# Kernel tuning notes

Hardware: AMD Instinct MI355X
Metric: run time of the kernel (lower is better)

Reference implementation:

```python
import jax, jax.numpy as jnp
import numpy as np

VOCAB, D, B, S, L, K = 50000, 256, 128, 64, 32, 32
EPS = 1e-12  # tf.nn.l2_normalize epsilon


def setup_inputs() -> dict:
    key = jax.random.key(0)
    ks = jax.random.split(key, 7)
    prgrph = jax.random.randint(ks[0], (B, S, L), 0, VOCAB, dtype=jnp.int32)
    prgrph_mask = jax.random.randint(ks[1], (B, S, L), 0, 2, dtype=jnp.int32).astype(bool)
    keys = jax.random.normal(ks[2], (B, K, D), dtype=jnp.float32)
    embedding_matrix = jax.random.normal(ks[3], (VOCAB, D), dtype=jnp.float32) * 0.05
    U = jax.random.normal(ks[4], (D, D), dtype=jnp.float32) * 0.05
    V = jax.random.normal(ks[5], (D, D), dtype=jnp.float32) * 0.05
    W = jax.random.normal(ks[6], (D, D), dtype=jnp.float32) * 0.05
    return {"prgrph": prgrph, "prgrph_mask": prgrph_mask, "keys": keys,
            "embedding_matrix": embedding_matrix, "U": U, "V": V, "W": W}


def reference(prgrph, prgrph_mask, keys, embedding_matrix, U, V, W):
    # bag-of-words sentence encoding: [B, S, L, D] -> sum over words -> [B, S, D]
    enc_sents = embedding_matrix[prgrph].sum(axis=2)
    sent_mask = prgrph_mask[:, :, 0]  # [B, S] sentence availability

    h0 = jnp.zeros_like(keys)  # initial entity hidden state [B, K, D]

    def step(h, inp):
        e, m = inp  # e: [B, D], m: [B] bool
        # gate_i = sigmoid(sum_d e * (h_i + k_i))  -> [B, K]
        gate = jax.nn.sigmoid(jnp.einsum('bd,bkd->bk', e, h + keys))
        # h_tilda = relu(h U + k V + e W)  -> [B, K, D]
        h_tilda = jax.nn.relu(
            jnp.einsum('bkd,de->bke', h, U)
            + jnp.einsum('bkd,de->bke', keys, V)
            + (e @ W)[:, None, :]
        )
        upd = h + gate[..., None] * h_tilda
        upd = upd * jax.lax.rsqrt(jnp.maximum((upd * upd).sum(-1, keepdims=True), EPS))
        h_new = jnp.where(m[:, None, None], upd, h)  # masked rows keep prev state
        return h_new, None

    h_final, _ = jax.lax.scan(step, h0, (enc_sents.transpose(1, 0, 2), sent_mask.T))
    return h_final  # [B, K, D]
```

## Files before the change

### kernel.cpp

```cpp
#include <hip/hip_runtime.h>

#define D 256
#define B 128
#define S 64
#define L 32
#define K 32
#define KH 16
#define NW 8
#define NSUB 2
#define HSTR 260

typedef _Float16 f16x8 __attribute__((ext_vector_type(8)));
typedef float f32x4 __attribute__((ext_vector_type(4)));
typedef unsigned short u16;

__device__ __forceinline__ u16 h_bits(_Float16 h) {
    union { _Float16 h; u16 u; } x; x.h = h; return x.u;
}

__global__ __launch_bounds__(256) void mask_kernel(const void* mraw, int* mask_out) {
    __shared__ int flag;
    const int tid = threadIdx.x;
    if (tid == 0) flag = 0;
    __syncthreads();
    const unsigned int* w32 = (const unsigned int*)mraw;
    int loc = 0;
    #pragma unroll
    for (int j = 0; j < 4; ++j)
        if (w32[tid * 4 + j] > 1u) loc = 1;
    if (loc) flag = 1;
    __syncthreads();
    const bool is_bytes = (flag != 0);
    const unsigned char* b8 = (const unsigned char*)mraw;
    const int* i32 = (const int*)mraw;
    const int i = blockIdx.x * 256 + tid;
    mask_out[i] = is_bytes ? (int)b8[(size_t)i * L] : i32[(size_t)i * L];
}

__global__ __launch_bounds__(256) void pre_kernel(
    const int* __restrict__ prgrph, const float* __restrict__ E,
    const float* __restrict__ Wm, const float* __restrict__ Vm,
    const float* __restrict__ keys, const int* __restrict__ mask,
    float* __restrict__ enc, float* __restrict__ eW,
    float* __restrict__ keysV, float* __restrict__ ek) {
    const int t = threadIdx.x, wave = t >> 6, lane = t & 63;
    __shared__ int   sidx[32][L];
    __shared__ float a_s[32][264];
    __shared__ float ks[32][260];

    const float* Bm;
    float* O;

    if (blockIdx.x < (B * S) / 32) {
        const int bid = blockIdx.x;
        const int b = bid >> 1;

        #pragma unroll
        for (int j = 0; j < 4; ++j) {
            const int idx = t * 4 + j;
            sidx[idx >> 5][idx & 31] = prgrph[(size_t)bid * 1024 + idx];
        }
        __syncthreads();

        const float4* E4 = (const float4*)E;
        for (int sl = wave * 8; sl < wave * 8 + 8; ++sl) {
            if (!mask[bid * 32 + sl]) continue;
            float4 a = make_float4(0.f, 0.f, 0.f, 0.f);
            #pragma unroll
            for (int l = 0; l < L; ++l) {
                const float4 v = E4[(size_t)sidx[sl][l] * (D / 4) + lane];
                a.x += v.x; a.y += v.y; a.z += v.z; a.w += v.w;
            }
            *(float4*)&a_s[sl][lane * 4] = a;
            *(float4*)&enc[(size_t)(bid * 32 + sl) * D + lane * 4] = a;
        }
        __syncthreads();
        Bm = Wm;
        O = eW + (size_t)bid * 32 * D;
    } else {
        const int row0 = (blockIdx.x - (B * S) / 32) * 32;
        const float4* Ag = (const float4*)(keys + (size_t)row0 * D);
        for (int i = t; i < 32 * D / 4; i += 256) {
            const float4 v = Ag[i];
            *(float4*)&a_s[i >> 6][(i & 63) * 4] = v;
        }
        __syncthreads();
        Bm = Vm;
        O = keysV + (size_t)row0 * D;
    }

    {
        const int r0 = wave * 8, c0 = lane * 4;
        float4 acc[8];
        #pragma unroll
        for (int i = 0; i < 8; ++i) acc[i] = make_float4(0.f, 0.f, 0.f, 0.f);
        for (int d = 0; d < D; d += 4) {
            float4 av[8];
            #pragma unroll
            for (int i = 0; i < 8; ++i) av[i] = *(const float4*)&a_s[r0 + i][d];
            #pragma unroll
            for (int j = 0; j < 4; ++j) {
                const float4 w = *(const float4*)(Bm + (size_t)(d + j) * D + c0);
                #pragma unroll
                for (int i = 0; i < 8; ++i) {
                    const float a = (j == 0) ? av[i].x : (j == 1) ? av[i].y
                                  : (j == 2) ? av[i].z : av[i].w;
                    acc[i].x += a * w.x; acc[i].y += a * w.y;
                    acc[i].z += a * w.z; acc[i].w += a * w.w;
                }
            }
        }
        #pragma unroll
        for (int i = 0; i < 8; ++i)
            *(float4*)&O[(size_t)(r0 + i) * D + c0] = acc[i];
    }

    if (blockIdx.x >= (B * S) / 32) return;

    {
        const int bid = blockIdx.x;
        const int b = bid >> 1;
        const float4* kg = (const float4*)(keys + (size_t)b * K * D);
        for (int i = t; i < K * D / 4; i += 256) {
            const float4 v = kg[i];
            *(float4*)&ks[i >> 6][(i & 63) * 4] = v;
        }
        __syncthreads();
        const int sl = t >> 3, kq = t & 7;
        if (mask[bid * 32 + sl]) {
            float acc[4];
            #pragma unroll
            for (int j = 0; j < 4; ++j) acc[j] = 0.f;
            for (int d4 = 0; d4 < D / 4; ++d4) {
                const float4 e = *(const float4*)&a_s[sl][d4 * 4];
                #pragma unroll
                for (int j = 0; j < 4; ++j) {
                    const float4 kv = *(const float4*)&ks[kq + 8 * j][d4 * 4];
                    acc[j] += e.x * kv.x + e.y * kv.y + e.z * kv.z + e.w * kv.w;
                }
            }
            #pragma unroll
            for (int j = 0; j < 4; ++j)
                ek[(size_t)(bid * 32 + sl) * K + kq + 8 * j] = acc[j];
        }
    }
}

__global__ __launch_bounds__(512, 2) void recur_kernel(
    const float* __restrict__ enc, const float* __restrict__ eWp,
    const float* __restrict__ keysV, const float* __restrict__ ek,
    const float* __restrict__ U, const int* __restrict__ mask,
    float* __restrict__ out) {
    const int b  = blockIdx.x >> 1;
    const int kh = (blockIdx.x & 1) * KH;
    const int t = threadIdx.x;
    const int wave = t >> 6, lane = t & 63;
    const int n = lane & 15, quad = lane >> 4;

    __shared__ u16 hF[2][KH][HSTR];
    __shared__ float redN[2][KH][NW];
    __shared__ float redG[2][KH][NW];

    f16x8 Uhi[NSUB][8], Ulo[NSUB][8];
    #pragma unroll
    for (int sub = 0; sub < NSUB; ++sub) {
        const int col = wave * 32 + sub * 16 + n;
        #pragma unroll
        for (int kt = 0; kt < 8; ++kt) {
            #pragma unroll
            for (int j = 0; j < 8; ++j) {
                const int k = kt * 32 + quad * 8 + j;
                const float u = U[(size_t)k * D + col];
                const _Float16 uh = (_Float16)u;
                Uhi[sub][kt][j] = uh;
                Ulo[sub][kt][j] = (_Float16)(u - (float)uh);
            }
        }
    }
    #pragma unroll
    for (int sub = 0; sub < NSUB; ++sub)
        #pragma unroll
        for (int kt = 0; kt < 8; ++kt)
            asm volatile("" : "+a"(Uhi[sub][kt]), "+a"(Ulo[sub][kt]));

    float upv[4][NSUB];
    float rn[4];
    float keysVc[4][NSUB];
    #pragma unroll
    for (int reg = 0; reg < 4; ++reg) {
        rn[reg] = 1.f;
        const size_t base = (size_t)(b * K + kh + quad * 4 + reg) * D;
        #pragma unroll
        for (int sub = 0; sub < NSUB; ++sub) {
            upv[reg][sub] = 0.f;
            keysVc[reg][sub] = keysV[base + wave * 32 + sub * 16 + n];
        }
    }

    const int* bm = mask + b * S;
    unsigned long long rem = __ballot(bm[lane & 63] != 0);

    float eWc[NSUB];
    float4 ekv = make_float4(0.f, 0.f, 0.f, 0.f);
    #pragma unroll
    for (int sub = 0; sub < NSUB; ++sub) eWc[sub] = 0.f;
    if (rem) {
        const int s0 = (int)__builtin_ctzll(rem);
        const size_t eo = (size_t)(b * S + s0) * D;
        #pragma unroll
        for (int sub = 0; sub < NSUB; ++sub)
            eWc[sub] = eWp[eo + wave * 32 + sub * 16 + n];
        ekv = *(const float4*)(ek + (size_t)(b * S + s0) * K + kh + quad * 4);
    }

    int p = 0, q = 0;
    bool first = true;
    while (rem) {
        rem &= rem - 1;
        const int sn = rem ? (int)__builtin_ctzll(rem) : -1;

        float e_n[NSUB];
        #pragma unroll
        for (int sub = 0; sub < NSUB; ++sub) e_n[sub] = 0.f;
        if (sn >= 0) {
            const size_t eo = (size_t)(b * S + sn) * D;
            #pragma unroll
            for (int sub = 0; sub < NSUB; ++sub)
                e_n[sub] = enc[eo + wave * 32 + sub * 16 + n];
        }

        f32x4 acc[NSUB][2];
        #pragma unroll
        for (int sub = 0; sub < NSUB; ++sub) {
            acc[sub][0] = (f32x4){0.f, 0.f, 0.f, 0.f};
            acc[sub][1] = (f32x4){0.f, 0.f, 0.f, 0.f};
        }
        if (!first) {
            #pragma unroll
            for (int kt = 0; kt < 8; ++kt) {
                const f16x8 av = *(const f16x8*)&hF[p][n][kt * 32 + quad * 8];
                #pragma unroll
                for (int sub = 0; sub < NSUB; ++sub) {
                    acc[sub][0] = __builtin_amdgcn_mfma_f32_16x16x32_f16(av, Uhi[sub][kt], acc[sub][0], 0, 0, 0);
                    acc[sub][1] = __builtin_amdgcn_mfma_f32_16x16x32_f16(av, Ulo[sub][kt], acc[sub][1], 0, 0, 0);
                }
            }
        }

        float gate[4];
        #pragma unroll
        for (int reg = 0; reg < 4; ++reg) {
            const float ekb = (reg == 0) ? ekv.x : (reg == 1) ? ekv.y
                            : (reg == 2) ? ekv.z : ekv.w;
            float g = ekb;
            if (!first) {
                const float* rg = redG[q ^ 1][quad * 4 + reg];
                const float4 g0 = *(const float4*)rg;
                const float4 g1 = *(const float4*)(rg + 4);
                g += rn[reg] * (g0.x + g0.y + g0.z + g0.w +
                                g1.x + g1.y + g1.z + g1.w);
            }
            gate[reg] = 1.f / (1.f + __expf(-g));
        }

        const int pw = p ^ 1;
        float pn[4], gd[4];
        #pragma unroll
        for (int reg = 0; reg < 4; ++reg) {
            const int row = quad * 4 + reg;
            float sq = 0.f, dv = 0.f;
            #pragma unroll
            for (int sub = 0; sub < NSUB; ++sub) {
                const float asum = acc[sub][0][reg] + acc[sub][1][reg];
                float ht = rn[reg] * asum + keysVc[reg][sub] + eWc[sub];
                ht = fmaxf(ht, 0.f);
                const float u2 = rn[reg] * upv[reg][sub] + gate[reg] * ht;
                upv[reg][sub] = u2;
                sq += u2 * u2;
                dv += u2 * e_n[sub];
                hF[pw][row][wave * 32 + sub * 16 + n] = h_bits((_Float16)u2);
            }
            pn[reg] = sq;
            gd[reg] = dv;
        }

        if (sn >= 0) {
            const size_t eo = (size_t)(b * S + sn) * D;
            #pragma unroll
            for (int sub = 0; sub < NSUB; ++sub)
                eWc[sub] = eWp[eo + wave * 32 + sub * 16 + n];
            ekv = *(const float4*)(ek + (size_t)(b * S + sn) * K + kh + quad * 4);
        }

        #pragma unroll
        for (int m = 1; m <= 8; m <<= 1) {
            #pragma unroll
            for (int reg = 0; reg < 4; ++reg) {
                pn[reg] += __shfl_xor(pn[reg], m);
                gd[reg] += __shfl_xor(gd[reg], m);
            }
        }
        if (n == 0) {
            #pragma unroll
            for (int reg = 0; reg < 4; ++reg) {
                redN[q][quad * 4 + reg][wave] = pn[reg];
                redG[q][quad * 4 + reg][wave] = gd[reg];
            }
        }

        __syncthreads();

        #pragma unroll
        for (int reg = 0; reg < 4; ++reg) {
            const float* rp = redN[q][quad * 4 + reg];
            const float4 r0 = *(const float4*)rp;
            const float4 r1 = *(const float4*)(rp + 4);
            rn[reg] = rsqrtf(fmaxf(r0.x + r0.y + r0.z + r0.w +
                                   r1.x + r1.y + r1.z + r1.w, 1e-12f));
        }
        p ^= 1; q ^= 1; first = false;
    }

    #pragma unroll
    for (int reg = 0; reg < 4; ++reg) {
        const size_t base = (size_t)(b * K + kh + quad * 4 + reg) * D;
        #pragma unroll
        for (int sub = 0; sub < NSUB; ++sub)
            out[base + wave * 32 + sub * 16 + n] = rn[reg] * upv[reg][sub];
    }
}

extern "C" void kernel_launch(void* const* d_in, const int* in_sizes, int n_in,
                              void* d_out, int out_size, void* d_ws, size_t ws_size,
                              hipStream_t stream) {
    const int*   prgrph = (const int*)d_in[0];
    const void*  pmask  = d_in[1];
    const float* keys   = (const float*)d_in[2];
    const float* E      = (const float*)d_in[3];
    const float* U      = (const float*)d_in[4];
    const float* V      = (const float*)d_in[5];
    const float* W      = (const float*)d_in[6];
    float* out = (float*)d_out;

    float* ws_enc   = (float*)d_ws;
    float* ws_eW    = ws_enc + (size_t)B * S * D;
    float* ws_keysV = ws_eW  + (size_t)B * S * D;
    float* ws_ek    = ws_keysV + (size_t)B * K * D;
    int*   ws_mask  = (int*)(ws_ek + (size_t)B * S * K);

    mask_kernel<<<32, 256, 0, stream>>>(pmask, ws_mask);
    pre_kernel<<<(B * S) / 32 + (B * K) / 32, 256, 0, stream>>>(
        prgrph, E, W, V, keys, ws_mask, ws_enc, ws_eW, ws_keysV, ws_ek);
    recur_kernel<<<B * (K / KH), 512, 0, stream>>>(
        ws_enc, ws_eW, ws_keysV, ws_ek, U, ws_mask, out);
}
```

Measured before the change: 238.4 us.

## Fuse mask conversion into pre-kernel and halve rows per block

Removes the separate mask_kernel launch by having each eW block detect the mask dtype and write its own slice of the int mask. Rows per block drop from 32 to 16, doubling the block count so more CUs are busy. The keys tile is no longer staged in shared memory for the ek dot products; keys are read straight from global. The trade-off is redundant dtype-detection reads in every block, and global instead of LDS reads for keys in the ek step.

```diff
diff --git a/kernel.cpp b/kernel.cpp
--- a/kernel.cpp
+++ b/kernel.cpp
@@ -18,53 +18,51 @@
     union { _Float16 h; u16 u; } x; x.h = h; return x.u;
 }
 
-__global__ __launch_bounds__(256) void mask_kernel(const void* mraw, int* mask_out) {
-    __shared__ int flag;
-    const int tid = threadIdx.x;
-    if (tid == 0) flag = 0;
-    __syncthreads();
-    const unsigned int* w32 = (const unsigned int*)mraw;
-    int loc = 0;
-    #pragma unroll
-    for (int j = 0; j < 4; ++j)
-        if (w32[tid * 4 + j] > 1u) loc = 1;
-    if (loc) flag = 1;
-    __syncthreads();
-    const bool is_bytes = (flag != 0);
-    const unsigned char* b8 = (const unsigned char*)mraw;
-    const int* i32 = (const int*)mraw;
-    const int i = blockIdx.x * 256 + tid;
-    mask_out[i] = is_bytes ? (int)b8[(size_t)i * L] : i32[(size_t)i * L];
-}
-
-__global__ __launch_bounds__(256) void pre_kernel(
+__global__ __launch_bounds__(256, 3) void pre_kernel(
     const int* __restrict__ prgrph, const float* __restrict__ E,
     const float* __restrict__ Wm, const float* __restrict__ Vm,
-    const float* __restrict__ keys, const int* __restrict__ mask,
+    const float* __restrict__ keys, const void* __restrict__ mraw,
     float* __restrict__ enc, float* __restrict__ eW,
-    float* __restrict__ keysV, float* __restrict__ ek) {
+    float* __restrict__ keysV, float* __restrict__ ek,
+    int* __restrict__ mask_out) {
     const int t = threadIdx.x, wave = t >> 6, lane = t & 63;
-    __shared__ int   sidx[32][L];
-    __shared__ float a_s[32][264];
-    __shared__ float ks[32][260];
-
+    __shared__ int   flag;
+    __shared__ int   smask[16];
+    __shared__ int   sidx[16][L];
+    __shared__ float a_s[16][264];
     const float* Bm;
     float* O;
-
-    if (blockIdx.x < (B * S) / 32) {
+    const bool is_eW = blockIdx.x < (B * S) / 16;
+
+    if (is_eW) {
         const int bid = blockIdx.x;
-        const int b = bid >> 1;
-
-        #pragma unroll
-        for (int j = 0; j < 4; ++j) {
-            const int idx = t * 4 + j;
-            sidx[idx >> 5][idx & 31] = prgrph[(size_t)bid * 1024 + idx];
-        }
-        __syncthreads();
-
+        const int b = bid >> 2;
+        if (t == 0) flag = 0;
+        __syncthreads();
+        const unsigned int* w32 = (const unsigned int*)mraw;
+        int loc = 0;
+        #pragma unroll
+        for (int j = 0; j < 4; ++j)
+            if (w32[t * 4 + j] > 1u) loc = 1;
+        if (loc) flag = 1;
+        #pragma unroll
+        for (int j = 0; j < 2; ++j) {
+            const int idx = t * 2 + j;
+            sidx[idx >> 5][idx & 31] = prgrph[(size_t)bid * (16 * L) + idx];
+        }
+        __syncthreads();
+        if (t < 16) {
+            const int gi = bid * 16 + t;
+            const int mv = (flag != 0)
+                ? (int)((const unsigned char*)mraw)[(size_t)gi * L]
+                : ((const int*)mraw)[(size_t)gi * L];
+            smask[t] = mv;
+            mask_out[gi] = mv;
+        }
+        __syncthreads();
         const float4* E4 = (const float4*)E;
-        for (int sl = wave * 8; sl < wave * 8 + 8; ++sl) {
-            if (!mask[bid * 32 + sl]) continue;
+        for (int sl = wave * 4; sl < wave * 4 + 4; ++sl) {
+            if (!smask[sl]) continue;
             float4 a = make_float4(0.f, 0.f, 0.f, 0.f);
             #pragma unroll
             for (int l = 0; l < L; ++l) {
@@ -72,37 +70,35 @@
                 a.x += v.x; a.y += v.y; a.z += v.z; a.w += v.w;
             }
             *(float4*)&a_s[sl][lane * 4] = a;
-            *(float4*)&enc[(size_t)(bid * 32 + sl) * D + lane * 4] = a;
+            *(float4*)&enc[(size_t)(bid * 16 + sl) * D + lane * 4] = a;
         }
         __syncthreads();
         Bm = Wm;
-        O = eW + (size_t)bid * 32 * D;
+        O = eW + (size_t)bid * 16 * D;
     } else {
-        const int row0 = (blockIdx.x - (B * S) / 32) * 32;
+        const int row0 = (blockIdx.x - (B * S) / 16) * 16;
         const float4* Ag = (const float4*)(keys + (size_t)row0 * D);
-        for (int i = t; i < 32 * D / 4; i += 256) {
-            const float4 v = Ag[i];
-            *(float4*)&a_s[i >> 6][(i & 63) * 4] = v;
-        }
+        for (int i = t; i < 16 * D / 4; i += 256)
+            *(float4*)&a_s[i >> 6][(i & 63) * 4] = Ag[i];
         __syncthreads();
         Bm = Vm;
         O = keysV + (size_t)row0 * D;
     }
 
     {
-        const int r0 = wave * 8, c0 = lane * 4;
-        float4 acc[8];
-        #pragma unroll
-        for (int i = 0; i < 8; ++i) acc[i] = make_float4(0.f, 0.f, 0.f, 0.f);
+        const int r0 = wave * 4, c0 = lane * 4;
+        float4 acc[4];
+        #pragma unroll
+        for (int i = 0; i < 4; ++i) acc[i] = make_float4(0.f, 0.f, 0.f, 0.f);
         for (int d = 0; d < D; d += 4) {
-            float4 av[8];
-            #pragma unroll
-            for (int i = 0; i < 8; ++i) av[i] = *(const float4*)&a_s[r0 + i][d];
+            float4 av[4];
+            #pragma unroll
+            for (int i = 0; i < 4; ++i) av[i] = *(const float4*)&a_s[r0 + i][d];
             #pragma unroll
             for (int j = 0; j < 4; ++j) {
                 const float4 w = *(const float4*)(Bm + (size_t)(d + j) * D + c0);
                 #pragma unroll
-                for (int i = 0; i < 8; ++i) {
+                for (int i = 0; i < 4; ++i) {
                     const float a = (j == 0) ? av[i].x : (j == 1) ? av[i].y
                                   : (j == 2) ? av[i].z : av[i].w;
                     acc[i].x += a * w.x; acc[i].y += a * w.y;
@@ -111,37 +107,28 @@
             }
         }
         #pragma unroll
-        for (int i = 0; i < 8; ++i)
+        for (int i = 0; i < 4; ++i)
             *(float4*)&O[(size_t)(r0 + i) * D + c0] = acc[i];
     }
 
-    if (blockIdx.x >= (B * S) / 32) return;
+    if (!is_eW) return;
 
     {
-        const int bid = blockIdx.x;
-        const int b = bid >> 1;
-        const float4* kg = (const float4*)(keys + (size_t)b * K * D);
-        for (int i = t; i < K * D / 4; i += 256) {
-            const float4 v = kg[i];
-            *(float4*)&ks[i >> 6][(i & 63) * 4] = v;
-        }
-        __syncthreads();
-        const int sl = t >> 3, kq = t & 7;
-        if (mask[bid * 32 + sl]) {
-            float acc[4];
-            #pragma unroll
-            for (int j = 0; j < 4; ++j) acc[j] = 0.f;
+        const int bid = blockIdx.x, b = bid >> 2;
+        const int sl = t >> 4, kq = t & 15;
+        if (smask[sl]) {
+            float acc0 = 0.f, acc1 = 0.f;
+            const float4* k0 = (const float4*)(keys + (size_t)(b * K + kq) * D);
+            const float4* k1 = (const float4*)(keys + (size_t)(b * K + kq + 16) * D);
             for (int d4 = 0; d4 < D / 4; ++d4) {
                 const float4 e = *(const float4*)&a_s[sl][d4 * 4];
-                #pragma unroll
-                for (int j = 0; j < 4; ++j) {
-                    const float4 kv = *(const float4*)&ks[kq + 8 * j][d4 * 4];
-                    acc[j] += e.x * kv.x + e.y * kv.y + e.z * kv.z + e.w * kv.w;
-                }
-            }
-            #pragma unroll
-            for (int j = 0; j < 4; ++j)
-                ek[(size_t)(bid * 32 + sl) * K + kq + 8 * j] = acc[j];
+                const float4 v0 = k0[d4];
+                const float4 v1 = k1[d4];
+                acc0 += e.x * v0.x + e.y * v0.y + e.z * v0.z + e.w * v0.w;
+                acc1 += e.x * v1.x + e.y * v1.y + e.z * v1.z + e.w * v1.w;
+            }
+            ek[(size_t)(bid * 16 + sl) * K + kq] = acc0;
+            ek[(size_t)(bid * 16 + sl) * K + kq + 16] = acc1;
         }
     }
 }
@@ -348,9 +335,8 @@
     float* ws_ek    = ws_keysV + (size_t)B * K * D;
     int*   ws_mask  = (int*)(ws_ek + (size_t)B * S * K);
 
-    mask_kernel<<<32, 256, 0, stream>>>(pmask, ws_mask);
-    pre_kernel<<<(B * S) / 32 + (B * K) / 32, 256, 0, stream>>>(
-        prgrph, E, W, V, keys, ws_mask, ws_enc, ws_eW, ws_keysV, ws_ek);
+    pre_kernel<<<(B * S) / 16 + (B * K) / 16, 256, 0, stream>>>(
+        prgrph, E, W, V, keys, pmask, ws_enc, ws_eW, ws_keysV, ws_ek, ws_mask);
     recur_kernel<<<B * (K / KH), 512, 0, stream>>>(
         ws_enc, ws_eW, ws_keysV, ws_ek, U, ws_mask, out);
 }
```

After: 258.0 us. 8.3% more time.

## Interleave recurrence columns per lane and use a transpose-style shuffle reduction

Applied to the files above, without the earlier changes.

Remaps each lane's two output columns from strided (n, n+16) to adjacent (2n, 2n+1) in the recurrent kernel. This turns the keysV, eW, enc and output accesses into float2 loads and stores, and the fp16 hidden-state LDS writes into one packed 32-bit store. The per-step norm and gate reductions are restructured into a butterfly that exchanges halves between lanes, cutting the shuffles from 32 to 8 per step before the block barrier. The risk is the extra select logic and the more intricate index mapping into the reduction buffers.

```diff
diff --git a/kernel.cpp b/kernel.cpp
--- a/kernel.cpp
+++ b/kernel.cpp
@@ -53,7 +53,6 @@
 
     if (blockIdx.x < (B * S) / 32) {
         const int bid = blockIdx.x;
-        const int b = bid >> 1;
 
         #pragma unroll
         for (int j = 0; j < 4; ++j) {
@@ -156,6 +155,7 @@
     const int t = threadIdx.x;
     const int wave = t >> 6, lane = t & 63;
     const int n = lane & 15, quad = lane >> 4;
+    const int col2 = wave * 32 + 2 * n;
 
     __shared__ u16 hF[2][KH][HSTR];
     __shared__ float redN[2][KH][NW];
@@ -164,7 +164,7 @@
     f16x8 Uhi[NSUB][8], Ulo[NSUB][8];
     #pragma unroll
     for (int sub = 0; sub < NSUB; ++sub) {
-        const int col = wave * 32 + sub * 16 + n;
+        const int col = col2 + sub;
         #pragma unroll
         for (int kt = 0; kt < 8; ++kt) {
             #pragma unroll
@@ -190,11 +190,9 @@
     for (int reg = 0; reg < 4; ++reg) {
         rn[reg] = 1.f;
         const size_t base = (size_t)(b * K + kh + quad * 4 + reg) * D;
-        #pragma unroll
-        for (int sub = 0; sub < NSUB; ++sub) {
-            upv[reg][sub] = 0.f;
-            keysVc[reg][sub] = keysV[base + wave * 32 + sub * 16 + n];
-        }
+        const float2 kv2 = *(const float2*)&keysV[base + col2];
+        keysVc[reg][0] = kv2.x; keysVc[reg][1] = kv2.y;
+        upv[reg][0] = 0.f; upv[reg][1] = 0.f;
     }
 
     const int* bm = mask + b * S;
@@ -202,14 +200,11 @@
 
     float eWc[NSUB];
     float4 ekv = make_float4(0.f, 0.f, 0.f, 0.f);
-    #pragma unroll
-    for (int sub = 0; sub < NSUB; ++sub) eWc[sub] = 0.f;
+    eWc[0] = 0.f; eWc[1] = 0.f;
     if (rem) {
         const int s0 = (int)__builtin_ctzll(rem);
-        const size_t eo = (size_t)(b * S + s0) * D;
-        #pragma unroll
-        for (int sub = 0; sub < NSUB; ++sub)
-            eWc[sub] = eWp[eo + wave * 32 + sub * 16 + n];
+        const float2 w2 = *(const float2*)&eWp[(size_t)(b * S + s0) * D + col2];
+        eWc[0] = w2.x; eWc[1] = w2.y;
         ekv = *(const float4*)(ek + (size_t)(b * S + s0) * K + kh + quad * 4);
     }
 
@@ -220,13 +215,10 @@
         const int sn = rem ? (int)__builtin_ctzll(rem) : -1;
 
         float e_n[NSUB];
-        #pragma unroll
-        for (int sub = 0; sub < NSUB; ++sub) e_n[sub] = 0.f;
+        e_n[0] = 0.f; e_n[1] = 0.f;
         if (sn >= 0) {
-            const size_t eo = (size_t)(b * S + sn) * D;
-            #pragma unroll
-            for (int sub = 0; sub < NSUB; ++sub)
-                e_n[sub] = enc[eo + wave * 32 + sub * 16 + n];
+            const float2 e2 = *(const float2*)&enc[(size_t)(b * S + sn) * D + col2];
+            e_n[0] = e2.x; e_n[1] = e2.y;
         }
 
         f32x4 acc[NSUB][2];
@@ -269,6 +261,7 @@
         for (int reg = 0; reg < 4; ++reg) {
             const int row = quad * 4 + reg;
             float sq = 0.f, dv = 0.f;
+            float u2s[2];
             #pragma unroll
             for (int sub = 0; sub < NSUB; ++sub) {
                 const float asum = acc[sub][0][reg] + acc[sub][1][reg];
@@ -276,35 +269,57 @@
                 ht = fmaxf(ht, 0.f);
                 const float u2 = rn[reg] * upv[reg][sub] + gate[reg] * ht;
                 upv[reg][sub] = u2;
+                u2s[sub] = u2;
                 sq += u2 * u2;
                 dv += u2 * e_n[sub];
-                hF[pw][row][wave * 32 + sub * 16 + n] = h_bits((_Float16)u2);
-            }
+            }
+            const unsigned int packed =
+                ((unsigned int)h_bits((_Float16)u2s[1]) << 16) |
+                (unsigned int)h_bits((_Float16)u2s[0]);
+            *(unsigned int*)&hF[pw][row][col2] = packed;
             pn[reg] = sq;
             gd[reg] = dv;
         }
 
         if (sn >= 0) {
-            const size_t eo = (size_t)(b * S + sn) * D;
-            #pragma unroll
-            for (int sub = 0; sub < NSUB; ++sub)
-                eWc[sub] = eWp[eo + wave * 32 + sub * 16 + n];
+            const float2 w2 = *(const float2*)&eWp[(size_t)(b * S + sn) * D + col2];
+            eWc[0] = w2.x; eWc[1] = w2.y;
             ekv = *(const float4*)(ek + (size_t)(b * S + sn) * K + kh + quad * 4);
         }
 
-        #pragma unroll
-        for (int m = 1; m <= 8; m <<= 1) {
-            #pragma unroll
-            for (int reg = 0; reg < 4; ++reg) {
-                pn[reg] += __shfl_xor(pn[reg], m);
-                gd[reg] += __shfl_xor(gd[reg], m);
-            }
-        }
-        if (n == 0) {
-            #pragma unroll
-            for (int reg = 0; reg < 4; ++reg) {
-                redN[q][quad * 4 + reg][wave] = pn[reg];
-                redG[q][quad * 4 + reg][wave] = gd[reg];
+        {
+            float v0 = pn[0], v1 = pn[1], v2 = pn[2], v3 = pn[3];
+            float w0 = gd[0], w1 = gd[1], w2 = gd[2], w3 = gd[3];
+            {
+                const bool hi = (n & 1);
+                float k0 = hi ? w0 : v0, x0 = hi ? v0 : w0;
+                float k1 = hi ? w1 : v1, x1 = hi ? v1 : w1;
+                float k2 = hi ? w2 : v2, x2 = hi ? v2 : w2;
+                float k3 = hi ? w3 : v3, x3 = hi ? v3 : w3;
+                v0 = k0 + __shfl_xor(x0, 1);
+                v1 = k1 + __shfl_xor(x1, 1);
+                v2 = k2 + __shfl_xor(x2, 1);
+                v3 = k3 + __shfl_xor(x3, 1);
+            }
+            {
+                const bool hi = (n & 2);
+                float k0 = hi ? v2 : v0, x0 = hi ? v0 : v2;
+                float k1 = hi ? v3 : v1, x1 = hi ? v1 : v3;
+                v0 = k0 + __shfl_xor(x0, 2);
+                v1 = k1 + __shfl_xor(x1, 2);
+            }
+            {
+                const bool hi = (n & 4);
+                float k0 = hi ? v1 : v0, x0 = hi ? v0 : v1;
+                v0 = k0 + __shfl_xor(x0, 4);
+            }
+            v0 += __shfl_xor(v0, 8);
+            if (n < 8) {
+                const int vid = ((n & 1) << 2) | (n & 2) | ((n >> 2) & 1);
+                const int row = quad * 4 + (vid & 3);
+                float* dst = (vid & 4) ? &redG[q][row][wave]
+                                       : &redN[q][row][wave];
+                *dst = v0;
             }
         }
 
@@ -324,9 +339,9 @@
     #pragma unroll
     for (int reg = 0; reg < 4; ++reg) {
         const size_t base = (size_t)(b * K + kh + quad * 4 + reg) * D;
-        #pragma unroll
-        for (int sub = 0; sub < NSUB; ++sub)
-            out[base + wave * 32 + sub * 16 + n] = rn[reg] * upv[reg][sub];
+        const float2 o2 = make_float2(rn[reg] * upv[reg][0],
+                                      rn[reg] * upv[reg][1]);
+        *(float2*)&out[base + col2] = o2;
     }
 }
 
```

Measured after the change: 218.8 us. -8.2%, faster.
